# Kernel optimization log

Measured on AMD Instinct MI355X. Metric: run time of the kernel, lower is better.

The kernel has to match this reference:

```python
import jax, jax.numpy as jnp
import numpy as np

NUM_PARAMS = 8          # number of generalized coordinates q
DIM = 2 * NUM_PARAMS    # state = (q, q_dot)
HID = 128               # hidden width of the Lagrangian MLP
BATCH = 4096


def _linear_init(key, fan_in, fan_out):
    # torch nn.Linear default init: U(-1/sqrt(fan_in), 1/sqrt(fan_in))
    lim = 1.0 / np.sqrt(fan_in)
    kw, kb = jax.random.split(key)
    W = jax.random.uniform(kw, (fan_out, fan_in), minval=-lim, maxval=lim, dtype=jnp.float32)
    b = jax.random.uniform(kb, (fan_out,), minval=-lim, maxval=lim, dtype=jnp.float32)
    return W, b


def setup_inputs() -> dict:
    key = jax.random.key(0)
    ks = jax.random.split(key, 6)
    W1, b1 = _linear_init(ks[0], DIM, HID)
    W2, b2 = _linear_init(ks[1], HID, HID)
    W3, b3 = _linear_init(ks[2], HID, HID)
    W4, b4 = _linear_init(ks[3], HID, HID)
    W5, b5 = _linear_init(ks[4], HID, 1)
    x = jax.random.normal(ks[5], (BATCH, DIM), dtype=jnp.float32)
    return {"x": x, "W1": W1, "b1": b1, "W2": W2, "b2": b2,
            "W3": W3, "b3": b3, "W4": W4, "b4": b4, "W5": W5, "b5": b5}


def reference(x, W1, b1, W2, b2, W3, b3, W4, b4, W5, b5):
    n = NUM_PARAMS

    def lagrangian(xs):  # xs: (DIM,) -> scalar L
        h = jax.nn.softplus(W1 @ xs + b1)
        h = jax.nn.softplus(W2 @ h + b2)
        h = jax.nn.softplus(W3 @ h + b3)
        h = jax.nn.softplus(W4 @ h + b4)
        return (W5 @ h + b5)[0]

    def per_sample(xs):
        J = jax.grad(lagrangian)(xs)            # (DIM,) = dL/dx
        H = jax.hessian(lagrangian)(xs)         # (DIM, DIM)
        A = J[:n]                               # dL/dq
        B = H[n:, n:]                           # d2L/dq_dot dq_dot
        C = H[n:, :n]                           # d2L/dq_dot dq
        # q_ddot = pinv(B) @ (dL/dq - d2L/dq_dot dq @ q_dot)
        return jnp.linalg.pinv(B) @ (A - C @ xs[n:])

    return jax.vmap(per_sample)(x)              # (BATCH, NUM_PARAMS)
```

## Files before the change

kernel.cpp:

```cpp
#include <hip/hip_runtime.h>
#include <math.h>

#define NPAR 8
#define DIM  16
#define HID  128
#define BATCH 4096
#define VSTRF 132
#define NVEC 9

typedef float v2f __attribute__((ext_vector_type(2)));
typedef float v4f __attribute__((ext_vector_type(4)));

#define PKFMA(d, a, b) asm("v_pk_fma_f32 %0, %1, %2, %0" : "+v"(d) : "v"(a), "v"(b))

__device__ float g_wsf[6*HID*HID + HID*DIM];

__device__ __forceinline__ float sigf(float z){ return 1.0f/(1.0f+__expf(-z)); }
__device__ __forceinline__ float spf(float z){ return fmaxf(z,0.0f)+log1pf(__expf(-fabsf(z))); }

__global__ __launch_bounds__(256)
void pack_weights(const float* __restrict__ W1, const float* __restrict__ W2,
                  const float* __restrict__ W3, const float* __restrict__ W4) {
  int t = blockIdx.x*blockDim.x + threadIdx.x;
  int p4 = t*4;
  float4 r;
  if (p4 < 6*HID*HID) {
    int ri = p4 >> 14;
    const float* W = (ri < 2) ? W2 : ((ri < 4) ? W3 : W4);
    int p  = p4 & 16383;
    int low = p & 127;
    int B  = p >> 7;
    int jo = (B & 3)*32 + (low >> 2);
    int T  = B >> 2;
    int kr0 = (T >> 4)*64 + (T & 15)*4;
    if ((ri & 1) == 0) {
      r = *((const float4*)(W + jo*HID + kr0));
    } else {
      r.x = W[(kr0+0)*HID + jo];
      r.y = W[(kr0+1)*HID + jo];
      r.z = W[(kr0+2)*HID + jo];
      r.w = W[(kr0+3)*HID + jo];
    }
  } else {
    int rr = p4 - 6*HID*HID;
    int k0 = (rr >> 6)*4;
    int m2 = (rr >> 2) & 15;
    r.x = W1[(k0+0)*DIM + m2];
    r.y = W1[(k0+1)*DIM + m2];
    r.z = W1[(k0+2)*DIM + m2];
    r.w = W1[(k0+3)*DIM + m2];
  }
  *((float4*)(g_wsf + p4)) = r;
}

__device__ __forceinline__ void gemv9f32(const float* __restrict__ Wbase,
    const float* __restrict__ bin, int o, int kh, float* zA, float* zB) {
  const v4f* Wq = (const v4f*)Wbase;
  const float* hb = bin + kh*64;
  v2f acc[4][NVEC];
#pragma unroll
  for (int jj=0;jj<4;++jj)
#pragma unroll
    for (int v=0;v<NVEC;++v) acc[jj][v] = (v2f){0.0f, 0.0f};
#pragma unroll 4
  for (int q=0;q<16;++q){
    int base = ((kh*16+q)*4)*32 + o;
    v4f w0 = Wq[base], w1 = Wq[base+32], w2 = Wq[base+64], w3 = Wq[base+96];
    v2f w0a=w0.xy, w0b=w0.zw;
    v2f w1a=w1.xy, w1b=w1.zw;
    v2f w2a=w2.xy, w2b=w2.zw;
    v2f w3a=w3.xy, w3b=w3.zw;
#pragma unroll
    for (int v=0;v<NVEC;++v){
      v4f h = *((const v4f*)(hb + v*VSTRF + 4*q));
      v2f ha=h.xy, hc=h.zw;
      PKFMA(acc[0][v], w0a, ha); PKFMA(acc[0][v], w0b, hc);
      PKFMA(acc[1][v], w1a, ha); PKFMA(acc[1][v], w1b, hc);
      PKFMA(acc[2][v], w2a, ha); PKFMA(acc[2][v], w2b, hc);
      PKFMA(acc[3][v], w3a, ha); PKFMA(acc[3][v], w3b, hc);
    }
  }
#pragma unroll
  for (int v=0;v<NVEC;++v){
    float u0 = acc[0][v].x + acc[0][v].y;
    float u1 = acc[1][v].x + acc[1][v].y;
    float u2 = acc[2][v].x + acc[2][v].y;
    float u3 = acc[3][v].x + acc[3][v].y;
    u0 += __shfl_xor(u0,32);
    u1 += __shfl_xor(u1,32);
    u2 += __shfl_xor(u2,32);
    u3 += __shfl_xor(u3,32);
    zA[v] = kh ? u2 : u0;
    zB[v] = kh ? u3 : u1;
  }
}

__global__ __launch_bounds__(64)
__attribute__((amdgpu_waves_per_eu(2)))
void lnn_main(const float* __restrict__ x, const float* __restrict__ W1,
              const float* __restrict__ b1, const float* __restrict__ b2,
              const float* __restrict__ b3, const float* __restrict__ b4,
              const float* __restrict__ W5, float* __restrict__ out) {
  const int l  = threadIdx.x;
  const int o  = l & 31;
  const int kh = l >> 5;
  const int ja = o + 64*kh;
  const int jb = ja + 32;
  const int s  = blockIdx.x;

  __shared__ __align__(16) float buf[NVEC*VSTRF];
  __shared__ float xs[16];

  if (l < DIM) xs[l] = x[s*DIM + l];
  __syncthreads();

  const float4* W1v = (const float4*)W1;
  float s1a, s1b;
  float w1af[8], w1bf[8];
  {
    float4 a0 = W1v[ja*4+0], a1 = W1v[ja*4+1], a2 = W1v[ja*4+2], a3 = W1v[ja*4+3];
    float4 c0 = W1v[jb*4+0], c1 = W1v[jb*4+1], c2 = W1v[jb*4+2], c3 = W1v[jb*4+3];
    float z1a = b1[ja], z1b = b1[jb];
    z1a = fmaf(a0.x, xs[0],  z1a); z1a = fmaf(a0.y, xs[1],  z1a);
    z1a = fmaf(a0.z, xs[2],  z1a); z1a = fmaf(a0.w, xs[3],  z1a);
    z1a = fmaf(a1.x, xs[4],  z1a); z1a = fmaf(a1.y, xs[5],  z1a);
    z1a = fmaf(a1.z, xs[6],  z1a); z1a = fmaf(a1.w, xs[7],  z1a);
    z1a = fmaf(a2.x, xs[8],  z1a); z1a = fmaf(a2.y, xs[9],  z1a);
    z1a = fmaf(a2.z, xs[10], z1a); z1a = fmaf(a2.w, xs[11], z1a);
    z1a = fmaf(a3.x, xs[12], z1a); z1a = fmaf(a3.y, xs[13], z1a);
    z1a = fmaf(a3.z, xs[14], z1a); z1a = fmaf(a3.w, xs[15], z1a);
    z1b = fmaf(c0.x, xs[0],  z1b); z1b = fmaf(c0.y, xs[1],  z1b);
    z1b = fmaf(c0.z, xs[2],  z1b); z1b = fmaf(c0.w, xs[3],  z1b);
    z1b = fmaf(c1.x, xs[4],  z1b); z1b = fmaf(c1.y, xs[5],  z1b);
    z1b = fmaf(c1.z, xs[6],  z1b); z1b = fmaf(c1.w, xs[7],  z1b);
    z1b = fmaf(c2.x, xs[8],  z1b); z1b = fmaf(c2.y, xs[9],  z1b);
    z1b = fmaf(c2.z, xs[10], z1b); z1b = fmaf(c2.w, xs[11], z1b);
    z1b = fmaf(c3.x, xs[12], z1b); z1b = fmaf(c3.y, xs[13], z1b);
    z1b = fmaf(c3.z, xs[14], z1b); z1b = fmaf(c3.w, xs[15], z1b);
    s1a = sigf(z1a); s1b = sigf(z1b);
    buf[ja] = spf(z1a); buf[jb] = spf(z1b);
    w1af[0]=a2.x; w1af[1]=a2.y; w1af[2]=a2.z; w1af[3]=a2.w;
    w1af[4]=a3.x; w1af[5]=a3.y; w1af[6]=a3.z; w1af[7]=a3.w;
    w1bf[0]=c2.x; w1bf[1]=c2.y; w1bf[2]=c2.z; w1bf[3]=c2.w;
    w1bf[4]=c3.x; w1bf[5]=c3.y; w1bf[6]=c3.z; w1bf[7]=c3.w;
#pragma unroll
    for (int i=0;i<8;++i){
      buf[(1+i)*VSTRF + ja] = s1a*w1af[i];
      buf[(1+i)*VSTRF + jb] = s1b*w1bf[i];
    }
  }
  __syncthreads();

  float zA[NVEC], zB[NVEC];

  gemv9f32(g_wsf + 0, buf, o, kh, zA, zB);
  float z2a = zA[0] + b2[ja], z2b = zB[0] + b2[jb];
  float t2a[8], t2b[8];
#pragma unroll
  for (int i=0;i<8;++i){ t2a[i]=zA[1+i]; t2b[i]=zB[1+i]; }
  float s2a = sigf(z2a), s2b = sigf(z2b);
  __syncthreads();
  buf[ja] = spf(z2a); buf[jb] = spf(z2b);
#pragma unroll
  for (int i=0;i<8;++i){
    buf[(1+i)*VSTRF + ja] = s2a*zA[1+i];
    buf[(1+i)*VSTRF + jb] = s2b*zB[1+i];
  }
  __syncthreads();

  gemv9f32(g_wsf + 32768, buf, o, kh, zA, zB);
  float z3a = zA[0] + b3[ja], z3b = zB[0] + b3[jb];
  float t3a[8], t3b[8];
#pragma unroll
  for (int i=0;i<8;++i){ t3a[i]=zA[1+i]; t3b[i]=zB[1+i]; }
  float s3a = sigf(z3a), s3b = sigf(z3b);
  __syncthreads();
  buf[ja] = spf(z3a); buf[jb] = spf(z3b);
#pragma unroll
  for (int i=0;i<8;++i){
    buf[(1+i)*VSTRF + ja] = s3a*zA[1+i];
    buf[(1+i)*VSTRF + jb] = s3b*zB[1+i];
  }
  __syncthreads();

  gemv9f32(g_wsf + 65536, buf, o, kh, zA, zB);
  {
    float z4a = zA[0] + b4[ja], z4b = zB[0] + b4[jb];
    float w5a = W5[ja], w5b = W5[jb];
    float sa = sigf(z4a), sb = sigf(z4b);
    float ca = w5a*sa*(1.0f-sa), cb = w5b*sb*(1.0f-sb);
    __syncthreads();
    buf[ja] = w5a*sa; buf[jb] = w5b*sb;
#pragma unroll
    for (int i=0;i<8;++i){
      buf[(1+i)*VSTRF + ja] = ca*zA[1+i];
      buf[(1+i)*VSTRF + jb] = cb*zB[1+i];
    }
  }
  __syncthreads();

  gemv9f32(g_wsf + 81920, buf, o, kh, zA, zB);
  {
    float da = s3a*(1.0f-s3a)*zA[0], db = s3b*(1.0f-s3b)*zB[0];
    __syncthreads();
    buf[ja] = zA[0]*s3a; buf[jb] = zB[0]*s3b;
#pragma unroll
    for (int i=0;i<8;++i){
      buf[(1+i)*VSTRF + ja] = fmaf(zA[1+i], s3a, da*t3a[i]);
      buf[(1+i)*VSTRF + jb] = fmaf(zB[1+i], s3b, db*t3b[i]);
    }
  }
  __syncthreads();

  gemv9f32(g_wsf + 49152, buf, o, kh, zA, zB);
  {
    float da = s2a*(1.0f-s2a)*zA[0], db = s2b*(1.0f-s2b)*zB[0];
    __syncthreads();
    buf[ja] = zA[0]*s2a; buf[jb] = zB[0]*s2b;
#pragma unroll
    for (int i=0;i<8;++i){
      buf[(1+i)*VSTRF + ja] = fmaf(zA[1+i], s2a, da*t2a[i]);
      buf[(1+i)*VSTRF + jb] = fmaf(zB[1+i], s2b, db*t2b[i]);
    }
  }
  __syncthreads();

  gemv9f32(g_wsf + 16384, buf, o, kh, zA, zB);
  {
    float da = s1a*(1.0f-s1a)*zA[0], db = s1b*(1.0f-s1b)*zB[0];
    __syncthreads();
    buf[ja] = zA[0]*s1a; buf[jb] = zB[0]*s1b;
#pragma unroll
    for (int i=0;i<8;++i){
      buf[(1+i)*VSTRF + ja] = fmaf(zA[1+i], s1a, da*w1af[i]);
      buf[(1+i)*VSTRF + jb] = fmaf(zB[1+i], s1b, db*w1bf[i]);
    }
  }
  __syncthreads();

  float hA, hB, hJ;
  {
    const int m = l & 15, d = l >> 4;
    const v4f* P1 = (const v4f*)(g_wsf + 98304);
    v2f aA={0.0f,0.0f}, aB={0.0f,0.0f}, aJ={0.0f,0.0f};
#pragma unroll 4
    for (int q=0; q<32; ++q){
      v4f wq = P1[q*DIM + m];
      v2f wa=wq.xy, wb=wq.zw;
      v4f u0 = *((const v4f*)(buf + (1+d)*VSTRF + 4*q));
      v4f u1 = *((const v4f*)(buf + (5+d)*VSTRF + 4*q));
      v4f gg = *((const v4f*)(buf + 4*q));
      PKFMA(aA, wa, u0.xy); PKFMA(aA, wb, u0.zw);
      PKFMA(aB, wa, u1.xy); PKFMA(aB, wb, u1.zw);
      PKFMA(aJ, wa, gg.xy); PKFMA(aJ, wb, gg.zw);
    }
    hA = aA.x + aA.y;
    hB = aB.x + aB.y;
    hJ = aJ.x + aJ.y;
  }

  {
    const int r = l >> 3, c = l & 7;
    float BvA = __shfl(hA, ((r&3)*16) + 8 + c);
    float BvB = __shfl(hB, ((r&3)*16) + 8 + c);
    float Bv  = (r < 4) ? BvA : BvB;
    float CrA = __shfl(hA, ((r&3)*16) + c);
    float CrB = __shfl(hB, ((r&3)*16) + c);
    float Cr  = (r < 4) ? CrA : CrB;
    float Jr  = __shfl(hJ, r);
    float p0 = Cr * xs[8 + c];
    p0 += __shfl_xor(p0, 1); p0 += __shfl_xor(p0, 2); p0 += __shfl_xor(p0, 4);
    float rhs = Jr - p0;

    float Bt = __shfl(Bv, c*8 + r);
    float Am = 0.5f*(Bv + Bt);
    float Vm = (r == c) ? 1.0f : 0.0f;

    for (int sweep = 0; sweep < 4; ++sweep) {
#pragma unroll
      for (int rr = 0; rr < 7; ++rr) {
        int pc = (c == 7) ? rr : ((c == rr) ? 7 : (2*rr + 7 - c) % 7);
        int cp = min(c, pc), cq = max(c, pc);
        float App = __shfl(Am, cp*8+cp);
        float Aqq = __shfl(Am, cq*8+cq);
        float Apq = __shfl(Am, cp*8+cq);
        float tau = (Aqq - App) / (2.0f*Apq);
        float tt  = (tau >= 0.0f ? 1.0f : -1.0f) / (fabsf(tau) + sqrtf(1.0f + tau*tau));
        float cth = 1.0f / sqrtf(1.0f + tt*tt);
        float sth = tt * cth;
        if (fabsf(Apq) < 1e-30f) { cth = 1.0f; sth = 0.0f; }
        float cthr = __shfl(cth, r*8+r);
        float sthr = __shfl(sth, r*8+r);
        float Arp = __shfl(Am, r*8+cp);
        float Arq = __shfl(Am, r*8+cq);
        float colv = (c == cp) ? (cth*Arp - sth*Arq) : (sth*Arp + cth*Arq);
        int pr2 = (r == 7) ? rr : ((r == rr) ? 7 : (2*rr + 7 - r) % 7);
        int rp = min(r, pr2), rq = max(r, pr2);
        float Mpc = __shfl(colv, rp*8+c);
        float Mqc = __shfl(colv, rq*8+c);
        Am = (r == rp) ? (cthr*Mpc - sthr*Mqc) : (sthr*Mpc + cthr*Mqc);
        float Vrp = __shfl(Vm, r*8+cp);
        float Vrq = __shfl(Vm, r*8+cq);
        Vm = (c == cp) ? (cth*Vrp - sth*Vrq) : (sth*Vrp + cth*Vrq);
      }
    }

    float lam_c = __shfl(Am, c*8 + c);
    float adiag = (r == c) ? fabsf(Am) : 0.0f;
#pragma unroll
    for (int off = 32; off; off >>= 1) adiag = fmaxf(adiag, __shfl_xor(adiag, off));
    float cutoff = 9.5367431640625e-06f * adiag;

    float pr = Vm * rhs;
    pr += __shfl_xor(pr, 8); pr += __shfl_xor(pr, 16); pr += __shfl_xor(pr, 32);
    float w = (fabsf(lam_c) > cutoff) ? (pr / lam_c) : 0.0f;
    float yr = Vm * w;
    yr += __shfl_xor(yr, 1); yr += __shfl_xor(yr, 2); yr += __shfl_xor(yr, 4);
    if (c == 0) out[s*NPAR + r] = yr;
  }
}

extern "C" void kernel_launch(void* const* d_in, const int* in_sizes, int n_in,
                              void* d_out, int out_size, void* d_ws, size_t ws_size,
                              hipStream_t stream) {
  (void)in_sizes; (void)n_in; (void)out_size; (void)d_ws; (void)ws_size;
  const float* x  = (const float*)d_in[0];
  const float* W1 = (const float*)d_in[1];
  const float* b1 = (const float*)d_in[2];
  const float* W2 = (const float*)d_in[3];
  const float* b2 = (const float*)d_in[4];
  const float* W3 = (const float*)d_in[5];
  const float* b3 = (const float*)d_in[6];
  const float* W4 = (const float*)d_in[7];
  const float* b4 = (const float*)d_in[8];
  const float* W5 = (const float*)d_in[9];
  float* out = (float*)d_out;

  pack_weights<<<98, 256, 0, stream>>>(W1, W2, W3, W4);
  lnn_main<<<BATCH, 64, 0, stream>>>(x, W1, b1, b2, b3, b4, W5, out);
}
```

Measured before the change: 224.0 us.

## Split per-sample work across two waves with 128-thread blocks

Each block now runs 128 threads (two wavefronts) instead of one, so each thread owns one hidden unit rather than two. This halves per-thread accumulators and weight loads in the gemv and raises the occupancy hint from 2 to 5 waves per EU. Because the Hessian rows now come from both waves, they are gathered through shared memory with an extra barrier before a single wave runs the Jacobi eigensolve. In exchange, barriers now span two waves, and the second wave sits idle during the eigensolve tail.

Result: no change. 227.1 us (+1.4%).

```diff
diff --git a/kernel.cpp b/kernel.cpp
--- a/kernel.cpp
+++ b/kernel.cpp
@@ -54,220 +54,173 @@
 }
 
 __device__ __forceinline__ void gemv9f32(const float* __restrict__ Wbase,
-    const float* __restrict__ bin, int o, int kh, float* zA, float* zB) {
+    const float* __restrict__ bin, int o, int kh, int w, float* z) {
   const v4f* Wq = (const v4f*)Wbase;
   const float* hb = bin + kh*64;
-  v2f acc[4][NVEC];
-#pragma unroll
-  for (int jj=0;jj<4;++jj)
-#pragma unroll
-    for (int v=0;v<NVEC;++v) acc[jj][v] = (v2f){0.0f, 0.0f};
-#pragma unroll 4
+  v2f acc0[NVEC], acc1[NVEC];
+#pragma unroll
+  for (int v=0;v<NVEC;++v){ acc0[v]=(v2f){0.0f,0.0f}; acc1[v]=(v2f){0.0f,0.0f}; }
+#pragma unroll 2
   for (int q=0;q<16;++q){
-    int base = ((kh*16+q)*4)*32 + o;
-    v4f w0 = Wq[base], w1 = Wq[base+32], w2 = Wq[base+64], w3 = Wq[base+96];
+    int base = ((kh*16+q)*4)*32 + w*64 + o;
+    v4f w0 = Wq[base], w1 = Wq[base+32];
     v2f w0a=w0.xy, w0b=w0.zw;
     v2f w1a=w1.xy, w1b=w1.zw;
-    v2f w2a=w2.xy, w2b=w2.zw;
-    v2f w3a=w3.xy, w3b=w3.zw;
 #pragma unroll
     for (int v=0;v<NVEC;++v){
       v4f h = *((const v4f*)(hb + v*VSTRF + 4*q));
       v2f ha=h.xy, hc=h.zw;
-      PKFMA(acc[0][v], w0a, ha); PKFMA(acc[0][v], w0b, hc);
-      PKFMA(acc[1][v], w1a, ha); PKFMA(acc[1][v], w1b, hc);
-      PKFMA(acc[2][v], w2a, ha); PKFMA(acc[2][v], w2b, hc);
-      PKFMA(acc[3][v], w3a, ha); PKFMA(acc[3][v], w3b, hc);
+      PKFMA(acc0[v], w0a, ha); PKFMA(acc0[v], w0b, hc);
+      PKFMA(acc1[v], w1a, ha); PKFMA(acc1[v], w1b, hc);
     }
   }
 #pragma unroll
   for (int v=0;v<NVEC;++v){
-    float u0 = acc[0][v].x + acc[0][v].y;
-    float u1 = acc[1][v].x + acc[1][v].y;
-    float u2 = acc[2][v].x + acc[2][v].y;
-    float u3 = acc[3][v].x + acc[3][v].y;
+    float u0 = acc0[v].x + acc0[v].y;
+    float u1 = acc1[v].x + acc1[v].y;
     u0 += __shfl_xor(u0,32);
     u1 += __shfl_xor(u1,32);
-    u2 += __shfl_xor(u2,32);
-    u3 += __shfl_xor(u3,32);
-    zA[v] = kh ? u2 : u0;
-    zB[v] = kh ? u3 : u1;
-  }
-}
-
-__global__ __launch_bounds__(64)
-__attribute__((amdgpu_waves_per_eu(2)))
+    z[v] = kh ? u1 : u0;
+  }
+}
+
+__global__ __launch_bounds__(128)
+__attribute__((amdgpu_waves_per_eu(5)))
 void lnn_main(const float* __restrict__ x, const float* __restrict__ W1,
               const float* __restrict__ b1, const float* __restrict__ b2,
               const float* __restrict__ b3, const float* __restrict__ b4,
               const float* __restrict__ W5, float* __restrict__ out) {
-  const int l  = threadIdx.x;
+  const int t  = threadIdx.x;
+  const int l  = t & 63;
   const int o  = l & 31;
   const int kh = l >> 5;
-  const int ja = o + 64*kh;
-  const int jb = ja + 32;
+  const int w  = t >> 6;
+  const int j  = w*64 + 32*kh + o;
   const int s  = blockIdx.x;
 
   __shared__ __align__(16) float buf[NVEC*VSTRF];
   __shared__ float xs[16];
-
-  if (l < DIM) xs[l] = x[s*DIM + l];
+  __shared__ float hH[8*16];
+  __shared__ float hJs[16];
+
+  if (t < DIM) xs[t] = x[s*DIM + t];
   __syncthreads();
 
   const float4* W1v = (const float4*)W1;
-  float s1a, s1b;
-  float w1af[8], w1bf[8];
-  {
-    float4 a0 = W1v[ja*4+0], a1 = W1v[ja*4+1], a2 = W1v[ja*4+2], a3 = W1v[ja*4+3];
-    float4 c0 = W1v[jb*4+0], c1 = W1v[jb*4+1], c2 = W1v[jb*4+2], c3 = W1v[jb*4+3];
-    float z1a = b1[ja], z1b = b1[jb];
-    z1a = fmaf(a0.x, xs[0],  z1a); z1a = fmaf(a0.y, xs[1],  z1a);
-    z1a = fmaf(a0.z, xs[2],  z1a); z1a = fmaf(a0.w, xs[3],  z1a);
-    z1a = fmaf(a1.x, xs[4],  z1a); z1a = fmaf(a1.y, xs[5],  z1a);
-    z1a = fmaf(a1.z, xs[6],  z1a); z1a = fmaf(a1.w, xs[7],  z1a);
-    z1a = fmaf(a2.x, xs[8],  z1a); z1a = fmaf(a2.y, xs[9],  z1a);
-    z1a = fmaf(a2.z, xs[10], z1a); z1a = fmaf(a2.w, xs[11], z1a);
-    z1a = fmaf(a3.x, xs[12], z1a); z1a = fmaf(a3.y, xs[13], z1a);
-    z1a = fmaf(a3.z, xs[14], z1a); z1a = fmaf(a3.w, xs[15], z1a);
-    z1b = fmaf(c0.x, xs[0],  z1b); z1b = fmaf(c0.y, xs[1],  z1b);
-    z1b = fmaf(c0.z, xs[2],  z1b); z1b = fmaf(c0.w, xs[3],  z1b);
-    z1b = fmaf(c1.x, xs[4],  z1b); z1b = fmaf(c1.y, xs[5],  z1b);
-    z1b = fmaf(c1.z, xs[6],  z1b); z1b = fmaf(c1.w, xs[7],  z1b);
-    z1b = fmaf(c2.x, xs[8],  z1b); z1b = fmaf(c2.y, xs[9],  z1b);
-    z1b = fmaf(c2.z, xs[10], z1b); z1b = fmaf(c2.w, xs[11], z1b);
-    z1b = fmaf(c3.x, xs[12], z1b); z1b = fmaf(c3.y, xs[13], z1b);
-    z1b = fmaf(c3.z, xs[14], z1b); z1b = fmaf(c3.w, xs[15], z1b);
-    s1a = sigf(z1a); s1b = sigf(z1b);
-    buf[ja] = spf(z1a); buf[jb] = spf(z1b);
-    w1af[0]=a2.x; w1af[1]=a2.y; w1af[2]=a2.z; w1af[3]=a2.w;
-    w1af[4]=a3.x; w1af[5]=a3.y; w1af[6]=a3.z; w1af[7]=a3.w;
-    w1bf[0]=c2.x; w1bf[1]=c2.y; w1bf[2]=c2.z; w1bf[3]=c2.w;
-    w1bf[4]=c3.x; w1bf[5]=c3.y; w1bf[6]=c3.z; w1bf[7]=c3.w;
-#pragma unroll
-    for (int i=0;i<8;++i){
-      buf[(1+i)*VSTRF + ja] = s1a*w1af[i];
-      buf[(1+i)*VSTRF + jb] = s1b*w1bf[i];
-    }
-  }
-  __syncthreads();
-
-  float zA[NVEC], zB[NVEC];
-
-  gemv9f32(g_wsf + 0, buf, o, kh, zA, zB);
-  float z2a = zA[0] + b2[ja], z2b = zB[0] + b2[jb];
-  float t2a[8], t2b[8];
-#pragma unroll
-  for (int i=0;i<8;++i){ t2a[i]=zA[1+i]; t2b[i]=zB[1+i]; }
-  float s2a = sigf(z2a), s2b = sigf(z2b);
-  __syncthreads();
-  buf[ja] = spf(z2a); buf[jb] = spf(z2b);
-#pragma unroll
-  for (int i=0;i<8;++i){
-    buf[(1+i)*VSTRF + ja] = s2a*zA[1+i];
-    buf[(1+i)*VSTRF + jb] = s2b*zB[1+i];
-  }
-  __syncthreads();
-
-  gemv9f32(g_wsf + 32768, buf, o, kh, zA, zB);
-  float z3a = zA[0] + b3[ja], z3b = zB[0] + b3[jb];
-  float t3a[8], t3b[8];
-#pragma unroll
-  for (int i=0;i<8;++i){ t3a[i]=zA[1+i]; t3b[i]=zB[1+i]; }
-  float s3a = sigf(z3a), s3b = sigf(z3b);
-  __syncthreads();
-  buf[ja] = spf(z3a); buf[jb] = spf(z3b);
-#pragma unroll
-  for (int i=0;i<8;++i){
-    buf[(1+i)*VSTRF + ja] = s3a*zA[1+i];
-    buf[(1+i)*VSTRF + jb] = s3b*zB[1+i];
-  }
-  __syncthreads();
-
-  gemv9f32(g_wsf + 65536, buf, o, kh, zA, zB);
-  {
-    float z4a = zA[0] + b4[ja], z4b = zB[0] + b4[jb];
-    float w5a = W5[ja], w5b = W5[jb];
-    float sa = sigf(z4a), sb = sigf(z4b);
-    float ca = w5a*sa*(1.0f-sa), cb = w5b*sb*(1.0f-sb);
-    __syncthreads();
-    buf[ja] = w5a*sa; buf[jb] = w5b*sb;
-#pragma unroll
-    for (int i=0;i<8;++i){
-      buf[(1+i)*VSTRF + ja] = ca*zA[1+i];
-      buf[(1+i)*VSTRF + jb] = cb*zB[1+i];
-    }
-  }
-  __syncthreads();
-
-  gemv9f32(g_wsf + 81920, buf, o, kh, zA, zB);
-  {
-    float da = s3a*(1.0f-s3a)*zA[0], db = s3b*(1.0f-s3b)*zB[0];
-    __syncthreads();
-    buf[ja] = zA[0]*s3a; buf[jb] = zB[0]*s3b;
-#pragma unroll
-    for (int i=0;i<8;++i){
-      buf[(1+i)*VSTRF + ja] = fmaf(zA[1+i], s3a, da*t3a[i]);
-      buf[(1+i)*VSTRF + jb] = fmaf(zB[1+i], s3b, db*t3b[i]);
-    }
-  }
-  __syncthreads();
-
-  gemv9f32(g_wsf + 49152, buf, o, kh, zA, zB);
-  {
-    float da = s2a*(1.0f-s2a)*zA[0], db = s2b*(1.0f-s2b)*zB[0];
-    __syncthreads();
-    buf[ja] = zA[0]*s2a; buf[jb] = zB[0]*s2b;
-#pragma unroll
-    for (int i=0;i<8;++i){
-      buf[(1+i)*VSTRF + ja] = fmaf(zA[1+i], s2a, da*t2a[i]);
-      buf[(1+i)*VSTRF + jb] = fmaf(zB[1+i], s2b, db*t2b[i]);
-    }
-  }
-  __syncthreads();
-
-  gemv9f32(g_wsf + 16384, buf, o, kh, zA, zB);
-  {
-    float da = s1a*(1.0f-s1a)*zA[0], db = s1b*(1.0f-s1b)*zB[0];
-    __syncthreads();
-    buf[ja] = zA[0]*s1a; buf[jb] = zB[0]*s1b;
-#pragma unroll
-    for (int i=0;i<8;++i){
-      buf[(1+i)*VSTRF + ja] = fmaf(zA[1+i], s1a, da*w1af[i]);
-      buf[(1+i)*VSTRF + jb] = fmaf(zB[1+i], s1b, db*w1bf[i]);
-    }
-  }
-  __syncthreads();
-
-  float hA, hB, hJ;
-  {
-    const int m = l & 15, d = l >> 4;
+  float s1;
+  float w1f[8];
+  {
+    float4 a0 = W1v[j*4+0], a1 = W1v[j*4+1], a2 = W1v[j*4+2], a3 = W1v[j*4+3];
+    float z1 = b1[j];
+    z1 = fmaf(a0.x, xs[0],  z1); z1 = fmaf(a0.y, xs[1],  z1);
+    z1 = fmaf(a0.z, xs[2],  z1); z1 = fmaf(a0.w, xs[3],  z1);
+    z1 = fmaf(a1.x, xs[4],  z1); z1 = fmaf(a1.y, xs[5],  z1);
+    z1 = fmaf(a1.z, xs[6],  z1); z1 = fmaf(a1.w, xs[7],  z1);
+    z1 = fmaf(a2.x, xs[8],  z1); z1 = fmaf(a2.y, xs[9],  z1);
+    z1 = fmaf(a2.z, xs[10], z1); z1 = fmaf(a2.w, xs[11], z1);
+    z1 = fmaf(a3.x, xs[12], z1); z1 = fmaf(a3.y, xs[13], z1);
+    z1 = fmaf(a3.z, xs[14], z1); z1 = fmaf(a3.w, xs[15], z1);
+    s1 = sigf(z1);
+    buf[j] = spf(z1);
+    w1f[0]=a2.x; w1f[1]=a2.y; w1f[2]=a2.z; w1f[3]=a2.w;
+    w1f[4]=a3.x; w1f[5]=a3.y; w1f[6]=a3.z; w1f[7]=a3.w;
+#pragma unroll
+    for (int i=0;i<8;++i) buf[(1+i)*VSTRF + j] = s1*w1f[i];
+  }
+  __syncthreads();
+
+  float z[NVEC];
+
+  gemv9f32(g_wsf + 0, buf, o, kh, w, z);
+  float z2 = z[0] + b2[j];
+  float t2[8];
+#pragma unroll
+  for (int i=0;i<8;++i) t2[i] = z[1+i];
+  float s2 = sigf(z2);
+  __syncthreads();
+  buf[j] = spf(z2);
+#pragma unroll
+  for (int i=0;i<8;++i) buf[(1+i)*VSTRF + j] = s2*z[1+i];
+  __syncthreads();
+
+  gemv9f32(g_wsf + 32768, buf, o, kh, w, z);
+  float z3 = z[0] + b3[j];
+  float t3[8];
+#pragma unroll
+  for (int i=0;i<8;++i) t3[i] = z[1+i];
+  float s3 = sigf(z3);
+  __syncthreads();
+  buf[j] = spf(z3);
+#pragma unroll
+  for (int i=0;i<8;++i) buf[(1+i)*VSTRF + j] = s3*z[1+i];
+  __syncthreads();
+
+  gemv9f32(g_wsf + 65536, buf, o, kh, w, z);
+  {
+    float z4 = z[0] + b4[j];
+    float w5 = W5[j];
+    float sa = sigf(z4);
+    float ca = w5*sa*(1.0f-sa);
+    __syncthreads();
+    buf[j] = w5*sa;
+#pragma unroll
+    for (int i=0;i<8;++i) buf[(1+i)*VSTRF + j] = ca*z[1+i];
+  }
+  __syncthreads();
+
+  gemv9f32(g_wsf + 81920, buf, o, kh, w, z);
+  {
+    float da = s3*(1.0f-s3)*z[0];
+    __syncthreads();
+    buf[j] = z[0]*s3;
+#pragma unroll
+    for (int i=0;i<8;++i) buf[(1+i)*VSTRF + j] = fmaf(z[1+i], s3, da*t3[i]);
+  }
+  __syncthreads();
+
+  gemv9f32(g_wsf + 49152, buf, o, kh, w, z);
+  {
+    float da = s2*(1.0f-s2)*z[0];
+    __syncthreads();
+    buf[j] = z[0]*s2;
+#pragma unroll
+    for (int i=0;i<8;++i) buf[(1+i)*VSTRF + j] = fmaf(z[1+i], s2, da*t2[i]);
+  }
+  __syncthreads();
+
+  gemv9f32(g_wsf + 16384, buf, o, kh, w, z);
+  {
+    float da = s1*(1.0f-s1)*z[0];
+    __syncthreads();
+    buf[j] = z[0]*s1;
+#pragma unroll
+    for (int i=0;i<8;++i) buf[(1+i)*VSTRF + j] = fmaf(z[1+i], s1, da*w1f[i]);
+  }
+  __syncthreads();
+
+  {
+    const int m = t & 15, dd = t >> 4;
     const v4f* P1 = (const v4f*)(g_wsf + 98304);
-    v2f aA={0.0f,0.0f}, aB={0.0f,0.0f}, aJ={0.0f,0.0f};
+    v2f aH={0.0f,0.0f}, aJ={0.0f,0.0f};
 #pragma unroll 4
     for (int q=0; q<32; ++q){
       v4f wq = P1[q*DIM + m];
       v2f wa=wq.xy, wb=wq.zw;
-      v4f u0 = *((const v4f*)(buf + (1+d)*VSTRF + 4*q));
-      v4f u1 = *((const v4f*)(buf + (5+d)*VSTRF + 4*q));
+      v4f u0 = *((const v4f*)(buf + (1+dd)*VSTRF + 4*q));
       v4f gg = *((const v4f*)(buf + 4*q));
-      PKFMA(aA, wa, u0.xy); PKFMA(aA, wb, u0.zw);
-      PKFMA(aB, wa, u1.xy); PKFMA(aB, wb, u1.zw);
+      PKFMA(aH, wa, u0.xy); PKFMA(aH, wb, u0.zw);
       PKFMA(aJ, wa, gg.xy); PKFMA(aJ, wb, gg.zw);
     }
-    hA = aA.x + aA.y;
-    hB = aB.x + aB.y;
-    hJ = aJ.x + aJ.y;
-  }
-
-  {
-    const int r = l >> 3, c = l & 7;
-    float BvA = __shfl(hA, ((r&3)*16) + 8 + c);
-    float BvB = __shfl(hB, ((r&3)*16) + 8 + c);
-    float Bv  = (r < 4) ? BvA : BvB;
-    float CrA = __shfl(hA, ((r&3)*16) + c);
-    float CrB = __shfl(hB, ((r&3)*16) + c);
-    float Cr  = (r < 4) ? CrA : CrB;
-    float Jr  = __shfl(hJ, r);
+    hH[dd*16 + m] = aH.x + aH.y;
+    if (dd == 0) hJs[m] = aJ.x + aJ.y;
+  }
+  __syncthreads();
+
+  if (t < 64) {
+    const int r = t >> 3, c = t & 7;
+    float Bv = hH[r*16 + 8 + c];
+    float Cr = hH[r*16 + c];
+    float Jr = hJs[r];
     float p0 = Cr * xs[8 + c];
     p0 += __shfl_xor(p0, 1); p0 += __shfl_xor(p0, 2); p0 += __shfl_xor(p0, 4);
     float rhs = Jr - p0;
@@ -313,8 +266,8 @@
 
     float pr = Vm * rhs;
     pr += __shfl_xor(pr, 8); pr += __shfl_xor(pr, 16); pr += __shfl_xor(pr, 32);
-    float w = (fabsf(lam_c) > cutoff) ? (pr / lam_c) : 0.0f;
-    float yr = Vm * w;
+    float ww = (fabsf(lam_c) > cutoff) ? (pr / lam_c) : 0.0f;
+    float yr = Vm * ww;
     yr += __shfl_xor(yr, 1); yr += __shfl_xor(yr, 2); yr += __shfl_xor(yr, 4);
     if (c == 0) out[s*NPAR + r] = yr;
   }
@@ -337,5 +290,5 @@
   float* out = (float*)d_out;
 
   pack_weights<<<98, 256, 0, stream>>>(W1, W2, W3, W4);
-  lnn_main<<<BATCH, 64, 0, stream>>>(x, W1, b1, b2, b3, b4, W5, out);
-}
+  lnn_main<<<BATCH, 128, 0, stream>>>(x, W1, b1, b2, b3, b4, W5, out);
+}
```
